# Performance work log

Hardware: AMD Instinct MI355X
Metric: run time of the kernel (lower is better)

Reference implementation:

```python
import jax, jax.numpy as jnp
import numpy as np

B, T, D = 8, 2048, 512
KQ, K = 32, 4  # DemandRouter defaults: k_query=32, k_topk=4


def setup_inputs() -> dict:
    key = jax.random.key(0)
    ks = jax.random.split(key, 9)

    def init(k, shape, fan_in):
        return (jax.random.normal(k, shape, jnp.float32) / np.sqrt(fan_in)).astype(jnp.float32)

    return dict(
        x=jax.random.normal(ks[0], (B, T, D), jnp.float32),
        # DemandRouter projections
        Wq=init(ks[1], (D, KQ), D), bq=jnp.zeros((KQ,), jnp.float32),
        Wk=init(ks[2], (D, KQ), D), bk=jnp.zeros((KQ,), jnp.float32),
        # System1 FFN (D -> 2D -> D) + LayerNorm
        W1=init(ks[3], (D, 2 * D), D), b1=jnp.zeros((2 * D,), jnp.float32),
        W2=init(ks[4], (2 * D, D), 2 * D), b2=jnp.zeros((D,), jnp.float32),
        ln_g=jnp.ones((D,), jnp.float32), ln_b=jnp.zeros((D,), jnp.float32),
        # System2 transform (2D -> 2D -> D)
        Wt1=init(ks[5], (2 * D, 2 * D), 2 * D), bt1=jnp.zeros((2 * D,), jnp.float32),
        Wt2=init(ks[6], (2 * D, D), 2 * D), bt2=jnp.zeros((D,), jnp.float32),
        # output projection
        Wo=init(ks[7], (D, D), D), bo=jnp.zeros((D,), jnp.float32),
    )


def reference(x, Wq, bq, Wk, bk, W1, b1, W2, b2, ln_g, ln_b, Wt1, bt1, Wt2, bt2, Wo, bo):
    # ---- DemandRouter: topk over query-key similarity, gather neighbors, mean ----
    q = x @ Wq + bq                      # [B,T,KQ]
    k = x @ Wk + bk                      # [B,T,KQ]
    sim = jnp.einsum('btk,bsk->bts', q, k) / np.float32(np.sqrt(KQ))  # [B,T,T]
    _, idx = jax.lax.top_k(sim, K)       # [B,T,K]
    # gather x[b, idx[b,t]] and mean over K neighbors -> [B,T,D]
    gathered = jax.vmap(lambda xb, ib: xb[ib])(x, idx).mean(axis=2)

    # ---- System1: residual FFN (exact GELU) + LayerNorm ----
    h = jax.nn.gelu(gathered @ W1 + b1, approximate=False) @ W2 + b2
    y = gathered + h
    mu = y.mean(-1, keepdims=True)
    var = y.var(-1, keepdims=True)
    y = (y - mu) / jnp.sqrt(var + 1e-5) * ln_g + ln_b  # [B,T,D]

    # ---- System2: sequential gated memory update over T ----
    def step(mem, xt):  # mem: [B,D], xt: [B,D]
        e = jnp.concatenate([xt, mem], axis=-1)                       # [B,2D]
        prop = jax.nn.gelu(e @ Wt1 + bt1, approximate=False) @ Wt2 + bt2  # [B,D]
        g = jax.nn.sigmoid(prop)
        mem = mem * (1.0 - g) + prop * g
        return mem, None

    mem0 = jnp.zeros((y.shape[0], y.shape[2]), y.dtype)
    mem_final, _ = jax.lax.scan(step, mem0, jnp.swapaxes(y, 0, 1))

    # pooled = system2_out[:, -1] == final memory
    return mem_final @ Wo + bo  # [B,D]
```

## Files before the change

### kernel.cpp

```cpp
#include <hip/hip_runtime.h>
#include <math.h>
#include <stdint.h>


using bf16x8 = __attribute__((ext_vector_type(8))) short;
using f32x4v = __attribute__((ext_vector_type(4))) float;
typedef unsigned long long ull;

__device__ inline unsigned short f2b(float f) {
  union { float f; unsigned int u; } v; v.f = f;
  unsigned int r = v.u + 0x7fffu + ((v.u >> 16) & 1u);
  return (unsigned short)(r >> 16);
}

__device__ inline float gelu_f(float x) {
  return 0.5f * x * (1.0f + erff(x * 0.70710678118654752f));
}

__device__ inline void ins4(float v, int i,
                            float& v0, int& i0, float& v1, int& i1,
                            float& v2, int& i2, float& v3, int& i3) {
  bool b0 = (v > v0) || (v == v0 && i < i0);
  bool b1 = (v > v1) || (v == v1 && i < i1);
  bool b2 = (v > v2) || (v == v2 && i < i2);
  bool b3 = (v > v3) || (v == v3 && i < i3);
  float nv3 = b2 ? v2 : (b3 ? v : v3); int ni3 = b2 ? i2 : (b3 ? i : i3);
  float nv2 = b1 ? v1 : (b2 ? v : v2); int ni2 = b1 ? i1 : (b2 ? i : i2);
  float nv1 = b0 ? v0 : (b1 ? v : v1); int ni1 = b0 ? i0 : (b1 ? i : i1);
  float nv0 = b0 ? v  : v0;            int ni0 = b0 ? i  : i0;
  v0=nv0; i0=ni0; v1=nv1; i1=ni1; v2=nv2; i2=ni2; v3=nv3; i3=ni3;
}


__global__ __launch_bounds__(256)
void wqk_kernel(const float* __restrict__ Wq, const float* __restrict__ Wk,
                float* __restrict__ wqk) {
  int id = blockIdx.x * 256 + threadIdx.x;
  int d = id >> 6, c = id & 63;
  wqk[id] = (c < 32) ? Wq[d * 32 + c] : Wk[d * 32 + (c - 32)];
}

__global__ __launch_bounds__(256)
void transpose_bf16_kernel(const float* __restrict__ src,
                           unsigned short* __restrict__ dst, int K, int N) {
  __shared__ float tile[32][33];
  int bk = blockIdx.x << 5, bn = blockIdx.y << 5;
  int c = threadIdx.x & 31, r8 = threadIdx.x >> 5;
  for (int r = r8; r < 32; r += 8) tile[r][c] = src[(size_t)(bk + r) * N + bn + c];
  __syncthreads();
  for (int r = r8; r < 32; r += 8) dst[(size_t)(bn + r) * K + bk + c] = f2b(tile[c][r]);
}


__global__ __launch_bounds__(256)
void qk_kernel(const float* __restrict__ x, const float* __restrict__ wqk,
               const float* __restrict__ bq, const float* __restrict__ bk,
               float* __restrict__ qkout) {
  __shared__ float xs[16][512];
  int tid = threadIdx.x;
  int b = blockIdx.x >> 7;
  int t0 = (blockIdx.x & 127) << 4;
  const float* xb = x + ((size_t)(b * 2048 + t0)) * 512;
#pragma unroll
  for (int i = 0; i < 8; ++i) {
    int f = i * 256 + tid;
    int r = f >> 7, c4 = f & 127;
    *(float4*)&xs[r][c4 * 4] = *(const float4*)&xb[(size_t)r * 512 + c4 * 4];
  }
  __syncthreads();
  int c = tid & 63, r4 = tid >> 6;
  float a0 = 0.f, a1 = 0.f, a2 = 0.f, a3 = 0.f;
#pragma unroll 4
  for (int d = 0; d < 512; ++d) {
    float w = wqk[d * 64 + c];
    a0 += xs[r4][d] * w;
    a1 += xs[r4 + 4][d] * w;
    a2 += xs[r4 + 8][d] * w;
    a3 += xs[r4 + 12][d] * w;
  }
  float bias = (c < 32) ? bq[c] : bk[c - 32];
  size_t base = ((size_t)(b * 2048 + t0)) * 64 + c;
  qkout[base + (size_t)r4 * 64] = a0 + bias;
  qkout[base + (size_t)(r4 + 4) * 64] = a1 + bias;
  qkout[base + (size_t)(r4 + 8) * 64] = a2 + bias;
  qkout[base + (size_t)(r4 + 12) * 64] = a3 + bias;
}

__global__ __launch_bounds__(256)
void topk_kernel(const float* __restrict__ qkb, int* __restrict__ idxout) {
  __shared__ float qs[16][36];
  __shared__ float ks[128][36];
  __shared__ float mv[16][16][4];
  __shared__ int   mi[16][16][4];
  int tid = threadIdx.x;
  int b = blockIdx.x >> 7;
  int t0 = (blockIdx.x & 127) << 4;
  const float* qb = qkb + ((size_t)b * 2048) * 64;
  if (tid < 128) {
    int r = tid >> 3, c4 = tid & 7;
    *(float4*)&qs[r][c4 * 4] = *(const float4*)&qb[(size_t)(t0 + r) * 64 + c4 * 4];
  }
  __syncthreads();
  int tl = tid >> 4, sl = tid & 15;
  float qv[32];
#pragma unroll
  for (int kk = 0; kk < 32; ++kk) qv[kk] = qs[tl][kk];
  float v0 = -INFINITY, v1 = -INFINITY, v2 = -INFINITY, v3 = -INFINITY;
  int i0 = 0x7fffffff, i1 = 0x7fffffff, i2 = 0x7fffffff, i3 = 0x7fffffff;
  for (int s0 = 0; s0 < 2048; s0 += 128) {
    __syncthreads();
#pragma unroll
    for (int p = 0; p < 4; ++p) {
      int f = p * 256 + tid;
      int r = f >> 3, c4 = f & 7;
      *(float4*)&ks[r][c4 * 4] =
          *(const float4*)&qb[(size_t)(s0 + r) * 64 + 32 + c4 * 4];
    }
    __syncthreads();
#pragma unroll
    for (int j = 0; j < 8; ++j) {
      int srow = j * 16 + sl;
      float accv = 0.f;
#pragma unroll
      for (int k4 = 0; k4 < 8; ++k4) {
        float4 kv = *(const float4*)&ks[srow][k4 * 4];
        accv += qv[k4 * 4 + 0] * kv.x + qv[k4 * 4 + 1] * kv.y +
                qv[k4 * 4 + 2] * kv.z + qv[k4 * 4 + 3] * kv.w;
      }
      ins4(accv, s0 + srow, v0, i0, v1, i1, v2, i2, v3, i3);
    }
  }
  mv[tl][sl][0] = v0; mv[tl][sl][1] = v1; mv[tl][sl][2] = v2; mv[tl][sl][3] = v3;
  mi[tl][sl][0] = i0; mi[tl][sl][1] = i1; mi[tl][sl][2] = i2; mi[tl][sl][3] = i3;
  __syncthreads();
  if (tid < 16) {
    float w0 = -INFINITY, w1 = -INFINITY, w2 = -INFINITY, w3 = -INFINITY;
    int a0 = 0x7fffffff, a1 = 0x7fffffff, a2 = 0x7fffffff, a3 = 0x7fffffff;
    for (int ss = 0; ss < 16; ++ss)
#pragma unroll
      for (int q = 0; q < 4; ++q)
        ins4(mv[tid][ss][q], mi[tid][ss][q], w0, a0, w1, a1, w2, a2, w3, a3);
    int4 o; o.x = a0; o.y = a1; o.z = a2; o.w = a3;
    *(int4*)&idxout[((size_t)(b * 2048 + t0 + tid)) * 4] = o;
  }
}

__global__ __launch_bounds__(128)
void gather_kernel(const float* __restrict__ x, const int* __restrict__ idx,
                   float* __restrict__ gf, unsigned short* __restrict__ gb) {
  int bt = blockIdx.x;
  int b = bt >> 11;
  const int4 iv = *(const int4*)&idx[(size_t)bt * 4];
  int tid = threadIdx.x;
  const float* xb = x + ((size_t)b * 2048) * 512;
  float4 p0 = *(const float4*)&xb[(size_t)iv.x * 512 + tid * 4];
  float4 p1 = *(const float4*)&xb[(size_t)iv.y * 512 + tid * 4];
  float4 p2 = *(const float4*)&xb[(size_t)iv.z * 512 + tid * 4];
  float4 p3 = *(const float4*)&xb[(size_t)iv.w * 512 + tid * 4];
  float4 m;
  m.x = (p0.x + p1.x + p2.x + p3.x) * 0.25f;
  m.y = (p0.y + p1.y + p2.y + p3.y) * 0.25f;
  m.z = (p0.z + p1.z + p2.z + p3.z) * 0.25f;
  m.w = (p0.w + p1.w + p2.w + p3.w) * 0.25f;
  *(float4*)&gf[(size_t)bt * 512 + tid * 4] = m;
  ushort4 u; u.x = f2b(m.x); u.y = f2b(m.y); u.z = f2b(m.z); u.w = f2b(m.w);
  *(ushort4*)&gb[(size_t)bt * 512 + tid * 4] = u;
}


template <int MODE>
__global__ __launch_bounds__(256, 2)
void gemm_bf16_k(const unsigned short* __restrict__ A,
                 const unsigned short* __restrict__ Bt,
                 const float* __restrict__ bias,
                 const float* __restrict__ resid,
                 void* __restrict__ outp, int M, int N, int K) {
  __shared__ unsigned short sA[128 * 32];
  __shared__ unsigned short sB[128 * 32];
  const int tid = threadIdx.x;
  const int lane = tid & 63, wave = tid >> 6;
  const int m0 = blockIdx.x * 128, n0 = blockIdx.y * 128;
  const int col16 = lane & 15, quad = lane >> 4;
  const int wm = wave >> 1, wn = wave & 1;
  f32x4v acc[4][4];
#pragma unroll
  for (int i = 0; i < 4; ++i)
#pragma unroll
    for (int j = 0; j < 4; ++j) {
      f32x4v z = {0.f, 0.f, 0.f, 0.f};
      acc[i][j] = z;
    }
  const int nkt = K >> 5;
  for (int kt = 0; kt < nkt; ++kt) {
    const int k0 = kt << 5;
#pragma unroll
    for (int p = 0; p < 2; ++p) {
      int f = p * 256 + tid;
      int row = f >> 2, q4 = f & 3;
      *(uint4*)&sA[row * 32 + q4 * 8] =
          *(const uint4*)(A + (size_t)(m0 + row) * K + k0 + q4 * 8);
      *(uint4*)&sB[row * 32 + q4 * 8] =
          *(const uint4*)(Bt + (size_t)(n0 + row) * K + k0 + q4 * 8);
    }
    __syncthreads();
    bf16x8 af[4], bfr[4];
#pragma unroll
    for (int i = 0; i < 4; ++i)
      af[i] = *(const bf16x8*)&sA[(wm * 64 + i * 16 + col16) * 32 + quad * 8];
#pragma unroll
    for (int j = 0; j < 4; ++j)
      bfr[j] = *(const bf16x8*)&sB[(wn * 64 + j * 16 + col16) * 32 + quad * 8];
#pragma unroll
    for (int i = 0; i < 4; ++i)
#pragma unroll
      for (int j = 0; j < 4; ++j)
        acc[i][j] = __builtin_amdgcn_mfma_f32_16x16x32_bf16(af[i], bfr[j],
                                                            acc[i][j], 0, 0, 0);
    __syncthreads();
  }
  float* outf = (float*)outp;
  unsigned short* outb = (unsigned short*)outp;
#pragma unroll
  for (int i = 0; i < 4; ++i)
#pragma unroll
    for (int j = 0; j < 4; ++j) {
      int col = n0 + wn * 64 + j * 16 + col16;
      float bs = bias[col];
#pragma unroll
      for (int r = 0; r < 4; ++r) {
        int row = m0 + wm * 64 + i * 16 + quad * 4 + r;
        float v = acc[i][j][r] + bs;
        if (MODE == 0) {
          outb[(size_t)row * N + col] = f2b(gelu_f(v));
        } else if (MODE == 1) {
          outf[(size_t)row * N + col] = v + resid[(size_t)row * N + col];
        } else {
          outf[(size_t)row * N + col] = v;
        }
      }
    }
}


__global__ __launch_bounds__(128)
void ln_kernel(const float* __restrict__ ypre, const float* __restrict__ lg,
               const float* __restrict__ lb, unsigned short* __restrict__ yb) {
  int row = blockIdx.x, tid = threadIdx.x;
  float4 v = *(const float4*)&ypre[(size_t)row * 512 + tid * 4];
  float s = v.x + v.y + v.z + v.w;
  float sq = v.x * v.x + v.y * v.y + v.z * v.z + v.w * v.w;
#pragma unroll
  for (int off = 1; off < 64; off <<= 1) {
    s += __shfl_xor(s, off, 64);
    sq += __shfl_xor(sq, off, 64);
  }
  __shared__ float red[4];
  if ((tid & 63) == 0) { red[(tid >> 6) * 2] = s; red[(tid >> 6) * 2 + 1] = sq; }
  __syncthreads();
  float S = red[0] + red[2], SQ = red[1] + red[3];
  float mu = S * (1.f / 512.f);
  float var = SQ * (1.f / 512.f) - mu * mu;
  float rstd = rsqrtf(var + 1e-5f);
  float4 g4 = *(const float4*)&lg[tid * 4];
  float4 b4 = *(const float4*)&lb[tid * 4];
  ushort4 u;
  u.x = f2b((v.x - mu) * rstd * g4.x + b4.x);
  u.y = f2b((v.y - mu) * rstd * g4.y + b4.y);
  u.z = f2b((v.z - mu) * rstd * g4.z + b4.z);
  u.w = f2b((v.w - mu) * rstd * g4.w + b4.w);
  *(ushort4*)&yb[(size_t)row * 512 + tid * 4] = u;
}


__global__ __launch_bounds__(256)
void system2_kernel(const float* __restrict__ Wt1, const float* __restrict__ Wt2,
                    const float* __restrict__ bt2, const float* __restrict__ xpart,
                    ull* __restrict__ gubuf, ull* __restrict__ membuf,
                    float* __restrict__ memfinal) {
  __shared__ float WbT[32 * 516];
  __shared__ float Wt2S[1024 * 16];
  __shared__ float guS[1024];
  __shared__ float memS[512];
  __shared__ float parts1[256];
  __shared__ float red2[256];

  const int t = threadIdx.x;
  const int team = blockIdx.x & 7;
  const int g = blockIdx.x >> 3;
  const int ucol0 = g << 5;
  const int mcol0 = g << 4;

  for (int idx = t; idx < 32 * 512; idx += 256) {
    int j = idx & 31, k = idx >> 5;
    WbT[j * 516 + k] = Wt1[(size_t)(512 + k) * 1024 + ucol0 + j];
  }
  for (int idx = t; idx < 1024 * 16; idx += 256) {
    int u = idx >> 4, dd = idx & 15;
    Wt2S[u * 16 + dd] = Wt2[(size_t)u * 512 + mcol0 + dd];
  }
  memS[t] = 0.f;
  memS[t + 256] = 0.f;
  const float bt2r = (t < 16) ? bt2[mcol0 + t] : 0.f;
  __syncthreads();

  const int j = t & 31, c = t >> 5;
  const int w = t >> 4, dd = t & 15;
  const bool skipown = (t >> 3) == g;
  const float* xp = xpart + (size_t)team * 2048 * 1024 + ucol0;
  float xv = (t < 32) ? xp[t] : 0.f;

  for (int s = 0; s < 2048; ++s) {
    const int par = s & 1;
    ull* gub = gubuf + (size_t)(par * 8 + team) * 1024;
    ull* memb = membuf + (size_t)(par * 8 + team) * 512;
    const ull tagv = (ull)(unsigned)(s + 1) << 32;

    float xnext = (t < 32 && s < 2047) ? xp[(size_t)(s + 1) * 1024 + t] : 0.f;

    {
      const float* wrow = &WbT[j * 516 + c * 64];
      const float* mrow = &memS[c * 64];
      float p1 = 0.f;
#pragma unroll
      for (int i = 0; i < 64; i += 4) {
        float4 wv = *(const float4*)&wrow[i];
        float4 mv = *(const float4*)&mrow[i];
        p1 += wv.x * mv.x + wv.y * mv.y + wv.z * mv.z + wv.w * mv.w;
      }
      parts1[c * 32 + j] = p1;
    }
    __syncthreads();
    if (t < 32) {
      float u = xv;
#pragma unroll
      for (int cc = 0; cc < 8; ++cc) u += parts1[cc * 32 + t];
      float gv = gelu_f(u);
      guS[ucol0 + t] = gv;
      union { float f; unsigned u32; } cv; cv.f = gv;
      __hip_atomic_store(&gub[ucol0 + t], tagv | cv.u32, __ATOMIC_RELAXED,
                         __HIP_MEMORY_SCOPE_AGENT);
    }
    if (!skipown) {
      const int u4 = t << 2;
      ull v0, v1, v2, v3;
      while (true) {
        v0 = __hip_atomic_load(&gub[u4 + 0], __ATOMIC_RELAXED,
                               __HIP_MEMORY_SCOPE_AGENT);
        v1 = __hip_atomic_load(&gub[u4 + 1], __ATOMIC_RELAXED,
                               __HIP_MEMORY_SCOPE_AGENT);
        v2 = __hip_atomic_load(&gub[u4 + 2], __ATOMIC_RELAXED,
                               __HIP_MEMORY_SCOPE_AGENT);
        v3 = __hip_atomic_load(&gub[u4 + 3], __ATOMIC_RELAXED,
                               __HIP_MEMORY_SCOPE_AGENT);
        bool ok = ((v0 >> 32) == (tagv >> 32)) && ((v1 >> 32) == (tagv >> 32)) &&
                  ((v2 >> 32) == (tagv >> 32)) && ((v3 >> 32) == (tagv >> 32));
        if (ok) break;
        __builtin_amdgcn_s_sleep(1);
      }
      union { unsigned u32; float f; } a;
      a.u32 = (unsigned)v0; guS[u4 + 0] = a.f;
      a.u32 = (unsigned)v1; guS[u4 + 1] = a.f;
      a.u32 = (unsigned)v2; guS[u4 + 2] = a.f;
      a.u32 = (unsigned)v3; guS[u4 + 3] = a.f;
    }
    __syncthreads();

    {
      float p2 = 0.f;
#pragma unroll
      for (int i = 0; i < 64; ++i) {
        const int u = i * 16 + w;
        p2 += guS[u] * Wt2S[u * 16 + dd];
      }
      red2[w * 16 + dd] = p2;
    }
    __syncthreads();
    if (t < 16) {
      float prop = bt2r;
#pragma unroll
      for (int ww = 0; ww < 16; ++ww) prop += red2[ww * 16 + t];
      float gate = 1.f / (1.f + __expf(-prop));
      float mnew = memS[mcol0 + t] * (1.f - gate) + prop * gate;
      memS[mcol0 + t] = mnew;
      union { float f; unsigned u32; } cv; cv.f = mnew;
      __hip_atomic_store(&memb[mcol0 + t], tagv | cv.u32, __ATOMIC_RELAXED,
                         __HIP_MEMORY_SCOPE_AGENT);
    }
    if (!skipown) {
      const int d2 = t << 1;
      ull v0, v1;
      while (true) {
        v0 = __hip_atomic_load(&memb[d2 + 0], __ATOMIC_RELAXED,
                               __HIP_MEMORY_SCOPE_AGENT);
        v1 = __hip_atomic_load(&memb[d2 + 1], __ATOMIC_RELAXED,
                               __HIP_MEMORY_SCOPE_AGENT);
        bool ok = ((v0 >> 32) == (tagv >> 32)) && ((v1 >> 32) == (tagv >> 32));
        if (ok) break;
        __builtin_amdgcn_s_sleep(1);
      }
      union { unsigned u32; float f; } a;
      a.u32 = (unsigned)v0; memS[d2 + 0] = a.f;
      a.u32 = (unsigned)v1; memS[d2 + 1] = a.f;
    }
    xv = xnext;
    __syncthreads();
  }

  if (g == 0 && t < 128)
    *(float4*)&memfinal[(size_t)team * 512 + t * 4] = *(float4*)&memS[t * 4];
}


__global__ __launch_bounds__(256)
void out_gemv_kernel(const float* __restrict__ memf, const float* __restrict__ Wo,
                     const float* __restrict__ bo, float* __restrict__ out) {
  int gid = blockIdx.x * 256 + threadIdx.x;
  int b = gid >> 9, d = gid & 511;
  const float* mb = memf + (size_t)b * 512;
  float acc = bo[d];
#pragma unroll 8
  for (int k = 0; k < 512; ++k) acc += mb[k] * Wo[(size_t)k * 512 + d];
  out[gid] = acc;
}


extern "C" void kernel_launch(void* const* d_in, const int* in_sizes, int n_in,
                              void* d_out, int out_size, void* d_ws, size_t ws_size,
                              hipStream_t stream) {
  const float* x   = (const float*)d_in[0];
  const float* Wq  = (const float*)d_in[1];
  const float* bq  = (const float*)d_in[2];
  const float* Wk  = (const float*)d_in[3];
  const float* bk  = (const float*)d_in[4];
  const float* W1  = (const float*)d_in[5];
  const float* b1  = (const float*)d_in[6];
  const float* W2  = (const float*)d_in[7];
  const float* b2  = (const float*)d_in[8];
  const float* lng = (const float*)d_in[9];
  const float* lnb = (const float*)d_in[10];
  const float* Wt1 = (const float*)d_in[11];
  const float* bt1 = (const float*)d_in[12];
  const float* Wt2 = (const float*)d_in[13];
  const float* bt2 = (const float*)d_in[14];
  const float* Wo  = (const float*)d_in[15];
  const float* bo  = (const float*)d_in[16];
  float* out = (float*)d_out;

  char* ws = (char*)d_ws;
  size_t off = 0;
  auto alloc = [&](size_t bytes) -> void* {
    void* p = ws + off;
    off += (bytes + 255) & ~(size_t)255;
    return p;
  };
  float* qk             = (float*)alloc(8ull * 2048 * 64 * 4);
  int* idxb             = (int*)alloc(8ull * 2048 * 4 * 4);
  float* gathf          = (float*)alloc(16384ull * 512 * 4);
  unsigned short* gathb = (unsigned short*)alloc(16384ull * 512 * 2);
  unsigned short* h1b   = (unsigned short*)alloc(16384ull * 1024 * 2);
  float* ypre           = (float*)alloc(16384ull * 512 * 4);
  unsigned short* yb    = (unsigned short*)alloc(16384ull * 512 * 2);
  float* xpart          = (float*)alloc(16384ull * 1024 * 4);
  unsigned short* w1t   = (unsigned short*)alloc(1024ull * 512 * 2);
  unsigned short* w2t   = (unsigned short*)alloc(512ull * 1024 * 2);
  unsigned short* wt1t  = (unsigned short*)alloc(1024ull * 512 * 2);
  float* wqkb           = (float*)alloc(512ull * 64 * 4);
  ull* gubuf            = (ull*)alloc(2ull * 8 * 1024 * 8);
  ull* membuf           = (ull*)alloc(2ull * 8 * 512 * 8);
  float* memf           = (float*)alloc(8ull * 512 * 4);
  if (off > ws_size) return;

  wqk_kernel<<<128, 256, 0, stream>>>(Wq, Wk, wqkb);
  transpose_bf16_kernel<<<dim3(16, 32), 256, 0, stream>>>(W1, w1t, 512, 1024);
  transpose_bf16_kernel<<<dim3(32, 16), 256, 0, stream>>>(W2, w2t, 1024, 512);
  transpose_bf16_kernel<<<dim3(16, 32), 256, 0, stream>>>(Wt1, wt1t, 512, 1024);

  qk_kernel<<<1024, 256, 0, stream>>>(x, wqkb, bq, bk, qk);
  topk_kernel<<<1024, 256, 0, stream>>>(qk, idxb);
  gather_kernel<<<16384, 128, 0, stream>>>(x, idxb, gathf, gathb);

  gemm_bf16_k<0><<<dim3(128, 8), 256, 0, stream>>>(gathb, w1t, b1, nullptr, h1b,
                                                   16384, 1024, 512);
  gemm_bf16_k<1><<<dim3(128, 4), 256, 0, stream>>>(h1b, w2t, b2, gathf, ypre,
                                                   16384, 512, 1024);
  ln_kernel<<<16384, 128, 0, stream>>>(ypre, lng, lnb, yb);
  gemm_bf16_k<2><<<dim3(128, 8), 256, 0, stream>>>(yb, wt1t, bt1, nullptr, xpart,
                                                   16384, 1024, 512);

  system2_kernel<<<256, 256, 0, stream>>>(Wt1, Wt2, bt2, xpart, gubuf, membuf,
                                          memf);
  out_gemv_kernel<<<16, 256, 0, stream>>>(memf, Wo, bo, out);
}
```

Before: 9.694 ms.

## Replace per-element tagged data polling with per-block flags and batch xpart prefetch

The cross-block exchange in the sequential scan no longer packs a step tag into every 64-bit value. Each block now stores plain floats, then publishes one flag per block. One wavefront polls the 32 flags with a ballot, after which the data is read once. The xpart input for 16 steps is also staged into shared memory in one batch rather than loaded per step. This is meant to cut polling traffic and per-step latency on the serial critical path. The cost is two extra block-wide barriers per phase, and correctness now depends on memory ordering between the relaxed data stores and the relaxed flag store, which has no release fence.

New measurement: 8.807 ms. 1.1x faster.

```diff
diff --git a/kernel.cpp b/kernel.cpp
--- a/kernel.cpp
+++ b/kernel.cpp
@@ -275,7 +275,8 @@
 __global__ __launch_bounds__(256)
 void system2_kernel(const float* __restrict__ Wt1, const float* __restrict__ Wt2,
                     const float* __restrict__ bt2, const float* __restrict__ xpart,
-                    ull* __restrict__ gubuf, ull* __restrict__ membuf,
+                    float* __restrict__ gubuf, float* __restrict__ membuf,
+                    int* __restrict__ flagA, int* __restrict__ flagB,
                     float* __restrict__ memfinal) {
   __shared__ float WbT[32 * 516];
   __shared__ float Wt2S[1024 * 16];
@@ -283,6 +284,7 @@
   __shared__ float memS[512];
   __shared__ float parts1[256];
   __shared__ float red2[256];
+  __shared__ float xbuf[16][32];
 
   const int t = threadIdx.x;
   const int team = blockIdx.x & 7;
@@ -301,21 +303,29 @@
   memS[t] = 0.f;
   memS[t + 256] = 0.f;
   const float bt2r = (t < 16) ? bt2[mcol0 + t] : 0.f;
-  __syncthreads();
 
   const int j = t & 31, c = t >> 5;
   const int w = t >> 4, dd = t & 15;
+  const int lane = t & 63;
   const bool skipown = (t >> 3) == g;
-  const float* xp = xpart + (size_t)team * 2048 * 1024 + ucol0;
-  float xv = (t < 32) ? xp[t] : 0.f;
+  const float* xpTeam = xpart + (size_t)team * 2048 * 1024 + ucol0;
+  const int ci = t >> 4, cp = (t & 15) << 1;
+  float2 cur2 = *(const float2*)&xpTeam[(size_t)ci * 1024 + cp];
+  __syncthreads();
 
   for (int s = 0; s < 2048; ++s) {
     const int par = s & 1;
-    ull* gub = gubuf + (size_t)(par * 8 + team) * 1024;
-    ull* memb = membuf + (size_t)(par * 8 + team) * 512;
-    const ull tagv = (ull)(unsigned)(s + 1) << 32;
-
-    float xnext = (t < 32 && s < 2047) ? xp[(size_t)(s + 1) * 1024 + t] : 0.f;
+    float* gub = gubuf + (size_t)(par * 8 + team) * 1024;
+    float* memb = membuf + (size_t)(par * 8 + team) * 512;
+    int* flA = flagA + (par * 8 + team) * 32;
+    int* flB = flagB + (par * 8 + team) * 32;
+    const int tagi = s + 1;
+
+    if ((s & 15) == 0) {
+      *(float2*)&xbuf[ci][cp] = cur2;
+      int ns = s + 16 + ci; if (ns > 2047) ns = 2047;
+      cur2 = *(const float2*)&xpTeam[(size_t)ns * 1024 + cp];
+    }
 
     {
       const float* wrow = &WbT[j * 516 + c * 64];
@@ -331,37 +341,40 @@
     }
     __syncthreads();
     if (t < 32) {
-      float u = xv;
+      float u = xbuf[s & 15][t];
 #pragma unroll
       for (int cc = 0; cc < 8; ++cc) u += parts1[cc * 32 + t];
       float gv = gelu_f(u);
       guS[ucol0 + t] = gv;
-      union { float f; unsigned u32; } cv; cv.f = gv;
-      __hip_atomic_store(&gub[ucol0 + t], tagv | cv.u32, __ATOMIC_RELAXED,
+      __hip_atomic_store(&gub[ucol0 + t], gv, __ATOMIC_RELAXED,
                          __HIP_MEMORY_SCOPE_AGENT);
     }
-    if (!skipown) {
-      const int u4 = t << 2;
-      ull v0, v1, v2, v3;
+    __syncthreads();
+    if (t == 0)
+      __hip_atomic_store(&flA[g], tagi, __ATOMIC_RELAXED,
+                         __HIP_MEMORY_SCOPE_AGENT);
+    {
+      const bool need = (lane < 32) && (lane != g);
+      const int* fp = &flA[lane & 31];
       while (true) {
-        v0 = __hip_atomic_load(&gub[u4 + 0], __ATOMIC_RELAXED,
-                               __HIP_MEMORY_SCOPE_AGENT);
-        v1 = __hip_atomic_load(&gub[u4 + 1], __ATOMIC_RELAXED,
-                               __HIP_MEMORY_SCOPE_AGENT);
-        v2 = __hip_atomic_load(&gub[u4 + 2], __ATOMIC_RELAXED,
-                               __HIP_MEMORY_SCOPE_AGENT);
-        v3 = __hip_atomic_load(&gub[u4 + 3], __ATOMIC_RELAXED,
-                               __HIP_MEMORY_SCOPE_AGENT);
-        bool ok = ((v0 >> 32) == (tagv >> 32)) && ((v1 >> 32) == (tagv >> 32)) &&
-                  ((v2 >> 32) == (tagv >> 32)) && ((v3 >> 32) == (tagv >> 32));
-        if (ok) break;
+        int f = need ? __hip_atomic_load(fp, __ATOMIC_RELAXED,
+                                         __HIP_MEMORY_SCOPE_AGENT)
+                     : tagi;
+        if (__ballot(f == tagi) == ~0ull) break;
         __builtin_amdgcn_s_sleep(1);
       }
-      union { unsigned u32; float f; } a;
-      a.u32 = (unsigned)v0; guS[u4 + 0] = a.f;
-      a.u32 = (unsigned)v1; guS[u4 + 1] = a.f;
-      a.u32 = (unsigned)v2; guS[u4 + 2] = a.f;
-      a.u32 = (unsigned)v3; guS[u4 + 3] = a.f;
+    }
+    __builtin_amdgcn_fence(__ATOMIC_ACQUIRE, "workgroup");
+    if (!skipown) {
+      const ull* gu64 = (const ull*)gub;
+      ull a = __hip_atomic_load(&gu64[2 * t], __ATOMIC_RELAXED,
+                                __HIP_MEMORY_SCOPE_AGENT);
+      ull b = __hip_atomic_load(&gu64[2 * t + 1], __ATOMIC_RELAXED,
+                                __HIP_MEMORY_SCOPE_AGENT);
+      guS[4 * t + 0] = __uint_as_float((unsigned)a);
+      guS[4 * t + 1] = __uint_as_float((unsigned)(a >> 32));
+      guS[4 * t + 2] = __uint_as_float((unsigned)b);
+      guS[4 * t + 3] = __uint_as_float((unsigned)(b >> 32));
     }
     __syncthreads();
 
@@ -382,27 +395,32 @@
       float gate = 1.f / (1.f + __expf(-prop));
       float mnew = memS[mcol0 + t] * (1.f - gate) + prop * gate;
       memS[mcol0 + t] = mnew;
-      union { float f; unsigned u32; } cv; cv.f = mnew;
-      __hip_atomic_store(&memb[mcol0 + t], tagv | cv.u32, __ATOMIC_RELAXED,
+      __hip_atomic_store(&memb[mcol0 + t], mnew, __ATOMIC_RELAXED,
                          __HIP_MEMORY_SCOPE_AGENT);
     }
-    if (!skipown) {
-      const int d2 = t << 1;
-      ull v0, v1;
+    __syncthreads();
+    if (t == 0)
+      __hip_atomic_store(&flB[g], tagi, __ATOMIC_RELAXED,
+                         __HIP_MEMORY_SCOPE_AGENT);
+    {
+      const bool need = (lane < 32) && (lane != g);
+      const int* fp = &flB[lane & 31];
       while (true) {
-        v0 = __hip_atomic_load(&memb[d2 + 0], __ATOMIC_RELAXED,
-                               __HIP_MEMORY_SCOPE_AGENT);
-        v1 = __hip_atomic_load(&memb[d2 + 1], __ATOMIC_RELAXED,
-                               __HIP_MEMORY_SCOPE_AGENT);
-        bool ok = ((v0 >> 32) == (tagv >> 32)) && ((v1 >> 32) == (tagv >> 32));
-        if (ok) break;
+        int f = need ? __hip_atomic_load(fp, __ATOMIC_RELAXED,
+                                         __HIP_MEMORY_SCOPE_AGENT)
+                     : tagi;
+        if (__ballot(f == tagi) == ~0ull) break;
         __builtin_amdgcn_s_sleep(1);
       }
-      union { unsigned u32; float f; } a;
-      a.u32 = (unsigned)v0; memS[d2 + 0] = a.f;
-      a.u32 = (unsigned)v1; memS[d2 + 1] = a.f;
-    }
-    xv = xnext;
+    }
+    __builtin_amdgcn_fence(__ATOMIC_ACQUIRE, "workgroup");
+    if (!skipown) {
+      const ull* mem64 = (const ull*)memb;
+      ull a = __hip_atomic_load(&mem64[t], __ATOMIC_RELAXED,
+                                __HIP_MEMORY_SCOPE_AGENT);
+      memS[2 * t + 0] = __uint_as_float((unsigned)a);
+      memS[2 * t + 1] = __uint_as_float((unsigned)(a >> 32));
+    }
     __syncthreads();
   }
 
@@ -465,8 +483,10 @@
   unsigned short* w2t   = (unsigned short*)alloc(512ull * 1024 * 2);
   unsigned short* wt1t  = (unsigned short*)alloc(1024ull * 512 * 2);
   float* wqkb           = (float*)alloc(512ull * 64 * 4);
-  ull* gubuf            = (ull*)alloc(2ull * 8 * 1024 * 8);
-  ull* membuf           = (ull*)alloc(2ull * 8 * 512 * 8);
+  float* gubuf          = (float*)alloc(2ull * 8 * 1024 * 4);
+  float* membuf         = (float*)alloc(2ull * 8 * 512 * 4);
+  int* flagA            = (int*)alloc(2ull * 8 * 32 * 4);
+  int* flagB            = (int*)alloc(2ull * 8 * 32 * 4);
   float* memf           = (float*)alloc(8ull * 512 * 4);
   if (off > ws_size) return;
 
@@ -488,6 +508,6 @@
                                                    16384, 1024, 512);
 
   system2_kernel<<<256, 256, 0, stream>>>(Wt1, Wt2, bt2, xpart, gubuf, membuf,
-                                          memf);
+                                          flagA, flagB, memf);
   out_gemv_kernel<<<16, 256, 0, stream>>>(memf, Wo, bo, out);
 }
```
